# Optimization experiments

Hardware: AMD Instinct MI355X
Metric: run time of the kernel (lower is better)

Reference implementation:

```python
import jax, jax.numpy as jnp
import numpy as np

NUM_HEADS = 12
HEIGHT = WIDTH = 24  # 24x24 patch grid + 1 cls token -> N = 577
NEG_INF = -65504.0


def _build_relative_position_index(height, width):
    # Faithful to MultiHeadRelativePositionalEmbedding.build (cls_token=True)
    num_relative_distance = (2 * height - 1) * (2 * width - 1) + 3
    hh, ww = np.meshgrid(range(height), range(width))
    coords = np.stack([hh, ww], axis=-1).reshape([-1, 2])
    rel = coords[:, None, :] - coords[None, :, :]
    rel_hh = rel[:, :, 0] + height - 1
    rel_ww = (rel[:, :, 1] + width - 1) * (2 * height - 1)
    idx = (rel_hh + rel_ww).astype('int64')  # [hw, hw]
    top = np.full((1, idx.shape[1]), num_relative_distance - 3, dtype=idx.dtype)
    left = np.full((idx.shape[0], 1), num_relative_distance - 2, dtype=idx.dtype)
    corner = np.full((1, 1), num_relative_distance - 1, dtype=idx.dtype)
    idx = np.concatenate([top, idx], axis=0)
    left_corner = np.concatenate([corner, left], axis=0)
    idx = np.concatenate([left_corner, idx], axis=1)  # [hw+1, hw+1]
    return idx.astype(np.int32)


def setup_inputs() -> dict:
    key = jax.random.key(0)
    ks = jax.random.split(key, 5)
    B, N, C = 16, HEIGHT * WIDTH + 1, 768
    nrd = (2 * HEIGHT - 1) * (2 * WIDTH - 1) + 3  # 2212
    x = jax.random.normal(ks[0], (B, N, C), dtype=jnp.float32)
    qkv_w = jax.random.normal(ks[1], (C, 3 * C), dtype=jnp.float32) * (C ** -0.5)
    qkv_b = jnp.zeros((3 * C,), dtype=jnp.float32)
    pos_emb = jax.random.normal(ks[2], (NUM_HEADS, nrd), dtype=jnp.float32) * 0.02
    out_w = jax.random.normal(ks[3], (C, C), dtype=jnp.float32) * (C ** -0.5)
    out_b = jnp.zeros((C,), dtype=jnp.float32)
    rel_index = jnp.asarray(_build_relative_position_index(HEIGHT, WIDTH))
    return {"x": x, "qkv_w": qkv_w, "qkv_b": qkv_b, "pos_emb": pos_emb,
            "out_w": out_w, "out_b": out_b, "rel_index": rel_index}


def reference(x, qkv_w, qkv_b, pos_emb, out_w, out_b, rel_index):
    B, N, C = x.shape
    H = NUM_HEADS
    d = C // H
    # QKV projection
    qkv = (x @ qkv_w + qkv_b).reshape(B, N, 3, H, d)
    q, k, v = [jnp.transpose(qkv[:, :, i], (0, 2, 1, 3)) for i in range(3)]  # [B,H,N,d]
    scale = jnp.asarray(d, x.dtype) ** -0.5
    attn = jnp.einsum('bhqd,bhkd->bhqk', q, k) * scale  # [B,H,N,N]
    # gathered relative-position bias: pos_emb[h, rel_index[q,k]] -> [H,N,N]
    bias = pos_emb[:, rel_index]
    # additive causal mask (CausalMask layer): (1 - tri(N)) * -65504
    mask = (1.0 - jnp.tri(N, dtype=x.dtype)) * NEG_INF
    attn = attn + bias[None] + mask[None, None]
    attn = jax.nn.softmax(attn, axis=-1)
    out = jnp.einsum('bhqk,bhkd->bhqd', attn, v)  # [B,H,N,d]
    out = jnp.transpose(out, (0, 2, 1, 3)).reshape(B, N, C)
    return out @ out_w + out_b
```

## Files before the change

### kernel.cpp

```cpp
#include <hip/hip_runtime.h>


#define BATCH 16
#define SEQ   577
#define CH    768
#define NH    12
#define HD    64
#define MROWS (BATCH*SEQ)
#define NRD   2212
#define NP    640
#define NPB   640

#define BM 128
#define BN 128
#define BK 64

typedef __attribute__((ext_vector_type(8))) short bf16x8;
typedef __attribute__((ext_vector_type(4))) float f32x4;
typedef const __attribute__((address_space(1))) unsigned int* gp_t;
typedef __attribute__((address_space(3))) unsigned int* lp_t;

static __device__ __forceinline__ unsigned short f2bf(float f) {
    unsigned int u = __float_as_uint(f);
    u = (u + 0x7FFFu + ((u >> 16) & 1u)) >> 16;
    return (unsigned short)u;
}
static __device__ __forceinline__ float bf2f(unsigned short b) {
    return __uint_as_float(((unsigned int)b) << 16);
}

#define CONV_NB 6924
#define TQ_NB   (72 * 24)
#define TO_NB   (24 * 24)
#define BIAS_NB 1600

__global__ __launch_bounds__(256) void prep_k(
    const float* __restrict__ x, unsigned short* __restrict__ xb,
    const float* __restrict__ qkv_w, unsigned short* __restrict__ qwt,
    const float* __restrict__ out_w, unsigned short* __restrict__ owt,
    const float* __restrict__ pos_emb, const int* __restrict__ rel_index,
    unsigned short* __restrict__ biasg)
{
    __shared__ float tile[32][33];
    const int t = threadIdx.x;
    int bid = blockIdx.x;

    if (bid < CONV_NB) {
        int i = bid * 256 + t;
        float4 v = ((const float4*)x)[i];
        ushort4 o;
        o.x = f2bf(v.x); o.y = f2bf(v.y); o.z = f2bf(v.z); o.w = f2bf(v.w);
        ((ushort4*)xb)[i] = o;
        return;
    }
    bid -= CONV_NB;
    if (bid < TQ_NB + TO_NB) {
        const float* w; unsigned short* wt; int K, N, nt;
        if (bid < TQ_NB) { w = qkv_w; wt = qwt; K = CH; N = 3 * CH; nt = 72; }
        else             { bid -= TQ_NB; w = out_w; wt = owt; K = CH; N = CH; nt = 24; }
        const int n0 = (bid % nt) * 32, k0 = (bid / nt) * 32;
        const int tx = t & 31, ty = t >> 5;
        #pragma unroll
        for (int i = 0; i < 32; i += 8)
            tile[ty + i][tx] = w[(size_t)(k0 + ty + i) * N + n0 + tx];
        __syncthreads();
        #pragma unroll
        for (int i = 0; i < 32; i += 8)
            wt[(size_t)(n0 + ty + i) * K + k0 + tx] = f2bf(tile[tx][ty + i]);
        return;
    }
    bid -= TQ_NB + TO_NB;
    {
        int i = bid * 256 + t;
        int q = i / NPB, k = i - q * NPB;
        const bool valid = (q < SEQ) & (k < SEQ);
        int idx = valid ? rel_index[q * SEQ + k] : 0;
        #pragma unroll
        for (int h = 0; h < NH; ++h)
            biasg[(size_t)h * NPB * NPB + i] =
                valid ? f2bf(pos_emb[h * NRD + idx]) : (unsigned short)0;
    }
}

__global__ __launch_bounds__(256) void vtrans_k(
    const unsigned short* __restrict__ v, unsigned short* __restrict__ vt)
{
    __shared__ unsigned short tile[64][68];
    const int bh = blockIdx.y;
    const int n0 = blockIdx.x * 64;
    const int tx = threadIdx.x & 7;
    const int ty = threadIdx.x >> 3;
    const unsigned short* src = v + ((size_t)bh * NP + n0) * HD;
    #pragma unroll
    for (int i = 0; i < 2; ++i) {
        int r = ty + i * 32;
        *(bf16x8*)&tile[r][tx * 8] = *(const bf16x8*)(src + (size_t)r * HD + tx * 8);
    }
    __syncthreads();
    unsigned short* dst = vt + (size_t)bh * HD * NP + n0;
    #pragma unroll
    for (int i = 0; i < 2; ++i) {
        int d = ty + i * 32;
        bf16x8 o;
        #pragma unroll
        for (int e = 0; e < 8; ++e) o[e] = (short)tile[tx * 8 + e][d];
        *(bf16x8*)(dst + (size_t)d * NP + tx * 8) = o;
    }
}

template<int MODE, int NNB, int NWG>
__global__ __launch_bounds__(256) void gemm_bf16_k(
    const unsigned short* __restrict__ A, const unsigned short* __restrict__ Bt,
    const float* __restrict__ bias, float* __restrict__ fo,
    unsigned short* __restrict__ qo, unsigned short* __restrict__ ko,
    unsigned short* __restrict__ vo, int Kdim)
{
    __shared__ unsigned short Asm[2][BM * BK];
    __shared__ unsigned short Bsm[2][BN * BK];
    const int t = threadIdx.x;
    const int wid = t >> 6, lane = t & 63;

    constexpr int Q = NWG / 8, R = NWG % 8;
    const int raw = blockIdx.x;
    const int xcd = raw & 7, idx = raw >> 3;
    const int wg = (xcd < R ? xcd * (Q + 1) : R * (Q + 1) + (xcd - R) * Q) + idx;
    const int m0 = (wg / NNB) * BM;
    const int n0 = (wg % NNB) * BN;

    const int wr = wid >> 1, wc = wid & 1;
    const int lr = lane & 15, lg = lane >> 4;
    const int swz = lr & 7;

    int srowA[4], ssegA[4];
    #pragma unroll
    for (int r = 0; r < 4; ++r) {
        int c = t + r * 256;
        srowA[r] = c >> 3;
        ssegA[r] = (c & 7) ^ ((c >> 3) & 7);
    }

    f32x4 acc[4][4] = {};

    auto stage = [&](int buf, int k0) {
        #pragma unroll
        for (int r = 0; r < 4; ++r) {
            int c = t + r * 256;
            int gm = m0 + srowA[r]; gm = gm < MROWS ? gm : MROWS - 1;
            __builtin_amdgcn_global_load_lds(
                (gp_t)(const void*)(A + (size_t)gm * Kdim + k0 + ssegA[r] * 8),
                (lp_t)(void*)(Asm[buf] + c * 8), 16, 0, 0);
        }
        #pragma unroll
        for (int r = 0; r < 4; ++r) {
            int c = t + r * 256;
            __builtin_amdgcn_global_load_lds(
                (gp_t)(const void*)(Bt + (size_t)(n0 + srowA[r]) * Kdim + k0 + ssegA[r] * 8),
                (lp_t)(void*)(Bsm[buf] + c * 8), 16, 0, 0);
        }
    };

    stage(0, 0);
    __syncthreads();

    const int NT = Kdim / BK;
    int cur = 0;
    for (int tt = 0; tt < NT; ++tt) {
        if (tt + 1 < NT) stage(cur ^ 1, (tt + 1) * BK);

        const unsigned short* Arow0 = Asm[cur] + (wr * 64 + lr) * BK;
        const unsigned short* Brow0 = Bsm[cur] + (wc * 64 + lr) * BK;
        #pragma unroll
        for (int kh = 0; kh < 2; ++kh) {
            const int goff = (((kh << 2) | lg) ^ swz) * 8;
            bf16x8 af[4], bfr[4];
            #pragma unroll
            for (int mi = 0; mi < 4; ++mi)
                af[mi] = *(const bf16x8*)(Arow0 + mi * 16 * BK + goff);
            #pragma unroll
            for (int ni = 0; ni < 4; ++ni)
                bfr[ni] = *(const bf16x8*)(Brow0 + ni * 16 * BK + goff);
            #pragma unroll
            for (int mi = 0; mi < 4; ++mi)
                #pragma unroll
                for (int ni = 0; ni < 4; ++ni)
                    acc[mi][ni] = __builtin_amdgcn_mfma_f32_16x16x32_bf16(
                        af[mi], bfr[ni], acc[mi][ni], 0, 0, 0);
        }
        __syncthreads();
        cur ^= 1;
    }

    const int gnb = n0 + wc * 64;
    float bs[4];
    #pragma unroll
    for (int ni = 0; ni < 4; ++ni) bs[ni] = bias[gnb + ni * 16 + lr];

    if (MODE == 0) {
        const int i3 = gnb / CH;
        const int hh = (gnb % CH) / HD;
        unsigned short* dst = (i3 == 0) ? qo : (i3 == 1) ? ko : vo;
        const float scl = (i3 == 0) ? 0.125f : 1.0f;
        #pragma unroll
        for (int mi = 0; mi < 4; ++mi) {
            #pragma unroll
            for (int j = 0; j < 4; ++j) {
                int gm = m0 + wr * 64 + mi * 16 + lg * 4 + j;
                if (gm < MROWS) {
                    int bb = gm / SEQ, ss = gm - bb * SEQ;
                    unsigned short* row =
                        dst + ((size_t)(bb * NH + hh) * NP + ss) * HD;
                    #pragma unroll
                    for (int ni = 0; ni < 4; ++ni)
                        row[ni * 16 + lr] = f2bf((acc[mi][ni][j] + bs[ni]) * scl);
                }
            }
        }
    } else {
        #pragma unroll
        for (int mi = 0; mi < 4; ++mi) {
            #pragma unroll
            for (int j = 0; j < 4; ++j) {
                int gm = m0 + wr * 64 + mi * 16 + lg * 4 + j;
                if (gm < MROWS) {
                    float* row = fo + (size_t)gm * CH + gnb;
                    #pragma unroll
                    for (int ni = 0; ni < 4; ++ni)
                        row[ni * 16 + lr] = acc[mi][ni][j] + bs[ni];
                }
            }
        }
    }
}

__global__ __launch_bounds__(256) void attn_mfma_k(
    const unsigned short* __restrict__ qg,
    const unsigned short* __restrict__ kg,
    const unsigned short* __restrict__ vtg,
    const unsigned short* __restrict__ biasg,
    unsigned short* __restrict__ out)
{
    __shared__ unsigned short Qs[64 * 64];
    __shared__ unsigned short Ks[64 * 64];
    __shared__ unsigned short VTs[64 * 64];
    __shared__ unsigned short Ps[64 * 64];
    __shared__ unsigned short Bs[64 * 64];

    constexpr int NWG = 1920, Qc = NWG / 8;
    const int raw = blockIdx.x;
    const int wg = (raw & 7) * Qc + (raw >> 3);
    const int qb = 9 - (wg % 10);
    const int y  = wg / 10;
    const int h  = y >> 4;
    const int b  = y & 15;
    const int bh = b * NH + h;

    const int t = threadIdx.x;
    const int wid = t >> 6;
    const int lane = t & 63;
    const int lr = lane & 15, lg = lane >> 4;
    const int q0 = qb * 64;

    const size_t kvbase = (size_t)bh * NP * HD;
    const size_t vtbase = (size_t)bh * HD * NP;
    const unsigned short* bbase = biasg + (size_t)h * NPB * NPB + (size_t)q0 * NPB;

    #pragma unroll
    for (int r = 0; r < 2; ++r) {
        int c = t + r * 256;
        int row = c >> 3, gsrc = (c & 7) ^ (row & 7);
        __builtin_amdgcn_global_load_lds(
            (gp_t)(const void*)(qg + kvbase + (size_t)(q0 + row) * HD + gsrc * 8),
            (lp_t)(void*)(Qs + c * 8), 16, 0, 0);
    }

    f32x4 o_acc[4] = {};
    float l_j[4] = {0.f, 0.f, 0.f, 0.f};

    const int qrow0 = q0 + wid * 16 + lg * 4;

    for (int kb = 0; kb <= qb; ++kb) {
        const int k0 = kb * 64;
        __syncthreads();
        #pragma unroll
        for (int r = 0; r < 2; ++r) {
            int c = t + r * 256;
            int row = c >> 3, gsrc = (c & 7) ^ (row & 7);
            __builtin_amdgcn_global_load_lds(
                (gp_t)(const void*)(kg + kvbase + (size_t)(k0 + row) * HD + gsrc * 8),
                (lp_t)(void*)(Ks + c * 8), 16, 0, 0);
        }
        #pragma unroll
        for (int r = 0; r < 2; ++r) {
            int c = t + r * 256;
            int row = c >> 3, gsrc = (c & 7) ^ (row & 7);
            __builtin_amdgcn_global_load_lds(
                (gp_t)(const void*)(vtg + vtbase + (size_t)row * NP + k0 + gsrc * 8),
                (lp_t)(void*)(VTs + c * 8), 16, 0, 0);
        }
        #pragma unroll
        for (int r = 0; r < 2; ++r) {
            int c = t + r * 256;
            int row = c >> 3, gsrc = (c & 7) ^ (row & 7);
            __builtin_amdgcn_global_load_lds(
                (gp_t)(const void*)(bbase + (size_t)row * NPB + k0 + gsrc * 8),
                (lp_t)(void*)(Bs + c * 8), 16, 0, 0);
        }
        __syncthreads();

        f32x4 s_acc[4] = {};
        #pragma unroll
        for (int kh = 0; kh < 2; ++kh) {
            const int arow = wid * 16 + lr;
            bf16x8 aq = *(const bf16x8*)(Qs + arow * 64 + ((((kh << 2) | lg)) ^ (arow & 7)) * 8);
            #pragma unroll
            for (int ni = 0; ni < 4; ++ni) {
                const int brow = ni * 16 + lr;
                bf16x8 bk = *(const bf16x8*)(Ks + brow * 64 + ((((kh << 2) | lg)) ^ (brow & 7)) * 8);
                s_acc[ni] = __builtin_amdgcn_mfma_f32_16x16x32_bf16(aq, bk, s_acc[ni], 0, 0, 0);
            }
        }

        float pv[4][4];
        #pragma unroll
        for (int j = 0; j < 4; ++j) {
            const int qrow = qrow0 + j;
            const int trow = wid * 16 + lg * 4 + j;
            float sum = 0.f;
            #pragma unroll
            for (int ni = 0; ni < 4; ++ni) {
                const int kcol = k0 + ni * 16 + lr;
                const int col = ni * 16 + lr;
                float v = s_acc[ni][j] +
                    bf2f(Bs[trow * 64 + (((col >> 3) ^ (trow & 7)) << 3) + (col & 7)]);
                float p = (kcol > qrow) ? 0.f : __expf(v);
                pv[ni][j] = p;
                sum += p;
            }
            l_j[j] += sum;
        }

        #pragma unroll
        for (int j = 0; j < 4; ++j) {
            const int prow = wid * 16 + lg * 4 + j;
            #pragma unroll
            for (int ni = 0; ni < 4; ++ni) {
                const int col = ni * 16 + lr;
                Ps[prow * 64 + (((col >> 3) ^ (prow & 7)) << 3) + (col & 7)] = f2bf(pv[ni][j]);
            }
        }
        __syncthreads();

        #pragma unroll
        for (int kh = 0; kh < 2; ++kh) {
            const int arow = wid * 16 + lr;
            bf16x8 pa = *(const bf16x8*)(Ps + arow * 64 + ((((kh << 2) | lg)) ^ (arow & 7)) * 8);
            #pragma unroll
            for (int ni = 0; ni < 4; ++ni) {
                const int brow = ni * 16 + lr;
                bf16x8 bv = *(const bf16x8*)(VTs + brow * 64 + ((((kh << 2) | lg)) ^ (brow & 7)) * 8);
                o_acc[ni] = __builtin_amdgcn_mfma_f32_16x16x32_bf16(pa, bv, o_acc[ni], 0, 0, 0);
            }
        }
    }

    #pragma unroll
    for (int j = 0; j < 4; ++j) {
        #pragma unroll
        for (int off = 1; off < 16; off <<= 1)
            l_j[j] += __shfl_xor(l_j[j], off, 64);
        const int qrow = qrow0 + j;
        if (qrow < SEQ) {
            const float inv = 1.0f / l_j[j];
            const size_t base = ((size_t)b * SEQ + qrow) * CH + h * HD;
            #pragma unroll
            for (int ni = 0; ni < 4; ++ni)
                out[base + ni * 16 + lr] = f2bf(o_acc[ni][j] * inv);
        }
    }
}

extern "C" void kernel_launch(void* const* d_in, const int* in_sizes, int n_in,
                              void* d_out, int out_size, void* d_ws, size_t ws_size,
                              hipStream_t stream) {
    const float* x        = (const float*)d_in[0];
    const float* qkv_w    = (const float*)d_in[1];
    const float* qkv_b    = (const float*)d_in[2];
    const float* pos_emb  = (const float*)d_in[3];
    const float* out_w    = (const float*)d_in[4];
    const float* out_b    = (const float*)d_in[5];
    const int*   rel_idx  = (const int*)d_in[6];
    float* out = (float*)d_out;

    const size_t QP = (size_t)BATCH * NH * NP * HD;
    unsigned short* qp  = (unsigned short*)d_ws;
    unsigned short* kp  = qp + QP;
    unsigned short* vp  = kp + QP;
    unsigned short* vt  = vp + QP;
    unsigned short* xb  = vt + QP;
    unsigned short* qwt = xb + (size_t)MROWS * CH;
    unsigned short* owt = qwt + (size_t)(3 * CH) * CH;
    unsigned short* bg  = owt + (size_t)CH * CH;

    prep_k<<<CONV_NB + TQ_NB + TO_NB + BIAS_NB, 256, 0, stream>>>(
        x, xb, qkv_w, qwt, out_w, owt, pos_emb, rel_idx, bg);

    gemm_bf16_k<0, 18, 1314><<<1314, 256, 0, stream>>>(
        xb, qwt, qkv_b, nullptr, qp, kp, vp, CH);

    vtrans_k<<<dim3(NP / 64, BATCH * NH), 256, 0, stream>>>(vp, vt);

    attn_mfma_k<<<1920, 256, 0, stream>>>(qp, kp, vt, bg, xb);

    gemm_bf16_k<1, 6, 438><<<438, 256, 0, stream>>>(
        xb, owt, out_b, out, nullptr, nullptr, nullptr, CH);
}
```

Baseline: 136.3 us.

## Keep Q in registers, read bias directly from global, add MFMA priority hints

The Q tile is loaded once into registers as MFMA operands, so its LDS buffer goes away. The bias tile is no longer staged through LDS and is instead read with per-lane global loads inside the softmax loop. s_setprio hints are placed around the MFMA sections. Together these cut LDS footprint (helping occupancy) and remove staging traffic, but the bias reads are now uncoalesced 2-byte global loads whose latency is exposed on the softmax path.

```diff
diff --git a/kernel.cpp b/kernel.cpp
--- a/kernel.cpp
+++ b/kernel.cpp
@@ -239,11 +239,9 @@
     const unsigned short* __restrict__ biasg,
     unsigned short* __restrict__ out)
 {
-    __shared__ unsigned short Qs[64 * 64];
     __shared__ unsigned short Ks[64 * 64];
     __shared__ unsigned short VTs[64 * 64];
     __shared__ unsigned short Ps[64 * 64];
-    __shared__ unsigned short Bs[64 * 64];
 
     constexpr int NWG = 1920, Qc = NWG / 8;
     const int raw = blockIdx.x;
@@ -262,16 +260,12 @@
 
     const size_t kvbase = (size_t)bh * NP * HD;
     const size_t vtbase = (size_t)bh * HD * NP;
-    const unsigned short* bbase = biasg + (size_t)h * NPB * NPB + (size_t)q0 * NPB;
-
-    #pragma unroll
-    for (int r = 0; r < 2; ++r) {
-        int c = t + r * 256;
-        int row = c >> 3, gsrc = (c & 7) ^ (row & 7);
-        __builtin_amdgcn_global_load_lds(
-            (gp_t)(const void*)(qg + kvbase + (size_t)(q0 + row) * HD + gsrc * 8),
-            (lp_t)(void*)(Qs + c * 8), 16, 0, 0);
-    }
+    const unsigned short* bb_p = biasg + (size_t)h * NPB * NPB + (size_t)q0 * NPB;
+
+    const int arow = wid * 16 + lr;
+    bf16x8 aq[2];
+    aq[0] = *(const bf16x8*)(qg + kvbase + (size_t)(q0 + arow) * HD + 0 + lg * 8);
+    aq[1] = *(const bf16x8*)(qg + kvbase + (size_t)(q0 + arow) * HD + 32 + lg * 8);
 
     f32x4 o_acc[4] = {};
     float l_j[4] = {0.f, 0.f, 0.f, 0.f};
@@ -297,41 +291,32 @@
                 (gp_t)(const void*)(vtg + vtbase + (size_t)row * NP + k0 + gsrc * 8),
                 (lp_t)(void*)(VTs + c * 8), 16, 0, 0);
         }
-        #pragma unroll
-        for (int r = 0; r < 2; ++r) {
-            int c = t + r * 256;
-            int row = c >> 3, gsrc = (c & 7) ^ (row & 7);
-            __builtin_amdgcn_global_load_lds(
-                (gp_t)(const void*)(bbase + (size_t)row * NPB + k0 + gsrc * 8),
-                (lp_t)(void*)(Bs + c * 8), 16, 0, 0);
-        }
         __syncthreads();
 
         f32x4 s_acc[4] = {};
+        __builtin_amdgcn_s_setprio(1);
         #pragma unroll
         for (int kh = 0; kh < 2; ++kh) {
-            const int arow = wid * 16 + lr;
-            bf16x8 aq = *(const bf16x8*)(Qs + arow * 64 + ((((kh << 2) | lg)) ^ (arow & 7)) * 8);
             #pragma unroll
             for (int ni = 0; ni < 4; ++ni) {
                 const int brow = ni * 16 + lr;
                 bf16x8 bk = *(const bf16x8*)(Ks + brow * 64 + ((((kh << 2) | lg)) ^ (brow & 7)) * 8);
-                s_acc[ni] = __builtin_amdgcn_mfma_f32_16x16x32_bf16(aq, bk, s_acc[ni], 0, 0, 0);
-            }
-        }
+                s_acc[ni] = __builtin_amdgcn_mfma_f32_16x16x32_bf16(aq[kh], bk, s_acc[ni], 0, 0, 0);
+            }
+        }
+        __builtin_amdgcn_s_setprio(0);
 
         float pv[4][4];
         #pragma unroll
         for (int j = 0; j < 4; ++j) {
             const int qrow = qrow0 + j;
             const int trow = wid * 16 + lg * 4 + j;
+            const unsigned short* brow = bb_p + (size_t)trow * NPB + k0;
             float sum = 0.f;
             #pragma unroll
             for (int ni = 0; ni < 4; ++ni) {
                 const int kcol = k0 + ni * 16 + lr;
-                const int col = ni * 16 + lr;
-                float v = s_acc[ni][j] +
-                    bf2f(Bs[trow * 64 + (((col >> 3) ^ (trow & 7)) << 3) + (col & 7)]);
+                float v = s_acc[ni][j] + bf2f(brow[ni * 16 + lr]);
                 float p = (kcol > qrow) ? 0.f : __expf(v);
                 pv[ni][j] = p;
                 sum += p;
@@ -350,9 +335,9 @@
         }
         __syncthreads();
 
+        __builtin_amdgcn_s_setprio(1);
         #pragma unroll
         for (int kh = 0; kh < 2; ++kh) {
-            const int arow = wid * 16 + lr;
             bf16x8 pa = *(const bf16x8*)(Ps + arow * 64 + ((((kh << 2) | lg)) ^ (arow & 7)) * 8);
             #pragma unroll
             for (int ni = 0; ni < 4; ++ni) {
@@ -361,6 +346,7 @@
                 o_acc[ni] = __builtin_amdgcn_mfma_f32_16x16x32_bf16(pa, bv, o_acc[ni], 0, 0, 0);
             }
         }
+        __builtin_amdgcn_s_setprio(0);
     }
 
     #pragma unroll
```

Result: faster. 133.1 us (-2.3%).
